# Kernel tuning notes

Measured on AMD Instinct MI355X. Metric: run time of the kernel, lower is better.

## Reference

```python
import jax, jax.numpy as jnp
import numpy as np


def setup_inputs() -> dict:
    key = jax.random.key(0)
    ks = jax.random.split(key, 24)
    N, C, D_IN, HID, EMB = 8192, 4096, 32, 128, 128
    s = 0.05
    inp = {
        "cand_feat": jax.random.normal(ks[0], (1, C, D_IN), jnp.float32),
        "graph_pos": jax.random.uniform(ks[1], (N, 3), jnp.float32),
        "graph_rad": jax.random.uniform(ks[2], (N,), jnp.float32) + 0.01,
        "L": jnp.ones((1,), jnp.float32),
        "adj": jax.random.uniform(ks[3], (N, N), jnp.float32),
        "mask": jax.random.randint(ks[4], (1, C), 0, 2, jnp.int32),
        # candidate encoder: 32 -> 128 -> 128
        "cW1": jax.random.normal(ks[5], (D_IN, 128), jnp.float32) * s,
        "cb1": jnp.zeros((128,), jnp.float32),
        "cW2": jax.random.normal(ks[6], (128, EMB), jnp.float32) * s,
        "cb2": jnp.zeros((EMB,), jnp.float32),
        # graph encoder input proj: 4 -> 128
        "gW0": jax.random.normal(ks[7], (4, HID), jnp.float32) * s,
        "gb0": jnp.zeros((HID,), jnp.float32),
        # 3 GNN layers: concat(2*HID) -> HID
        "gnnW": jax.random.normal(ks[8], (3, 2 * HID, HID), jnp.float32) * s,
        "gnnb": jnp.zeros((3, HID), jnp.float32),
        # output proj: 2*HID -> EMB
        "goW": jax.random.normal(ks[9], (2 * HID, EMB), jnp.float32) * s,
        "gob": jnp.zeros((EMB,), jnp.float32),
        # fusion: 2*EMB -> 256 -> 128 -> 1
        "fW1": jax.random.normal(ks[10], (2 * EMB, 256), jnp.float32) * s,
        "fb1": jnp.zeros((256,), jnp.float32),
        "fW2": jax.random.normal(ks[11], (256, 128), jnp.float32) * s,
        "fb2": jnp.zeros((128,), jnp.float32),
        "fW3": jax.random.normal(ks[12], (128, 1), jnp.float32) * s,
        "fb3": jnp.zeros((1,), jnp.float32),
    }
    return inp


def reference(cand_feat, graph_pos, graph_rad, L, adj, mask,
              cW1, cb1, cW2, cb2, gW0, gb0, gnnW, gnnb, goW, gob,
              fW1, fb1, fW2, fb2, fW3, fb3):
    relu = jax.nn.relu
    # ---- candidate encoder: [1, C, 32] -> [1, C, 128]
    cand_emb = relu(relu(cand_feat @ cW1 + cb1) @ cW2 + cb2)
    # ---- graph encoder ----
    node = jnp.concatenate([graph_pos / L, (graph_rad / jnp.max(graph_rad))[:, None]], axis=1)  # [N, 4]
    h = relu(node @ gW0 + gb0)  # [N, HID]
    deg = jnp.clip(jnp.sum(adj, axis=-1, keepdims=True), 1.0)  # [N, 1]
    for i in range(gnnW.shape[0]):
        agg = (adj @ h) / deg                       # degree-normalized aggregation
        h = relu(jnp.concatenate([h, agg], axis=-1) @ gnnW[i] + gnnb[i])
    h_glob = jnp.concatenate([jnp.max(h, axis=0), jnp.mean(h, axis=0)], axis=-1)  # [2*HID]
    graph_emb = h_glob @ goW + gob  # [EMB]
    # ---- fusion decoder ----
    g_exp = jnp.broadcast_to(graph_emb[None, None, :], cand_emb.shape)
    combined = jnp.concatenate([cand_emb, g_exp], axis=-1)  # [1, C, 2*EMB]
    scores = (relu(relu(combined @ fW1 + fb1) @ fW2 + fb2) @ fW3 + fb3)[..., 0]  # [1, C]
    return jnp.where(mask == 0, -jnp.inf, scores)
```

## Files before the change

kernel.cpp:

```cpp
#include <hip/hip_runtime.h>
#include <hip/hip_bf16.h>

constexpr int NN  = 8192;
constexpr int CC  = 4096;
constexpr int HD  = 128;
constexpr int KSPLIT = 8;
constexpr int KCHUNK = NN / KSPLIT;
constexpr int KSTEPS = KCHUNK / 64;

typedef __attribute__((ext_vector_type(8))) short bf16x8;
typedef __attribute__((ext_vector_type(4))) short s16x4;
typedef __attribute__((ext_vector_type(4))) float f32x4;

static __device__ __forceinline__ unsigned short f2bf(float f) {
  unsigned int u = __builtin_bit_cast(unsigned int, f);
  unsigned int lsb = (u >> 16) & 1u;
  u += 0x7fffu + lsb;
  return (unsigned short)(u >> 16);
}
static __device__ __forceinline__ float bf2f(unsigned short u) {
  return __builtin_bit_cast(float, ((unsigned int)u) << 16);
}

static __device__ __forceinline__ int swz(int r, int k) {
  return r * 128 + ((((k >> 3) ^ (r & 7))) << 4) + ((k & 7) * 2);
}

#define GL16(gp, lp)                                                              \
  __builtin_amdgcn_global_load_lds(                                               \
      (const __attribute__((address_space(1))) void*)(gp),                        \
      (__attribute__((address_space(3))) void*)(lp), 16, 0, 0)

__global__ __launch_bounds__(256) void k_radmax(const float* __restrict__ rad, float* out) {
  __shared__ float red[256];
  int t = threadIdx.x;
  float m = 0.0f;
  for (int i = t; i < NN; i += 256) m = fmaxf(m, rad[i]);
  red[t] = m; __syncthreads();
  for (int s = 128; s > 0; s >>= 1) {
    if (t < s) red[t] = fmaxf(red[t], red[t + s]);
    __syncthreads();
  }
  if (t == 0) out[0] = red[0];
}

__global__ __launch_bounds__(256) void k_h0(const float* __restrict__ pos, const float* __restrict__ rad,
                                            const float* __restrict__ Lp, const float* __restrict__ rmax,
                                            const float* __restrict__ gW0, const float* __restrict__ gb0,
                                            float* __restrict__ h, unsigned short* __restrict__ hT) {
  __shared__ __align__(16) unsigned short lt[128][72];
  int t = threadIdx.x;
  int i0 = blockIdx.x * 64;
  float invL = 1.0f / Lp[0];
  float invR = 1.0f / rmax[0];
  for (int rep = 0; rep < 32; ++rep) {
    int idx = rep * 256 + t;
    int il = idx >> 7, j = idx & 127;
    int i = i0 + il;
    float n0 = pos[i * 3 + 0] * invL, n1 = pos[i * 3 + 1] * invL, n2 = pos[i * 3 + 2] * invL;
    float n3 = rad[i] * invR;
    float v = gb0[j] + n0 * gW0[j] + n1 * gW0[128 + j] + n2 * gW0[256 + j] + n3 * gW0[384 + j];
    v = fmaxf(v, 0.0f);
    h[(size_t)i * HD + j] = v;
    lt[j][il] = f2bf(v);
  }
  __syncthreads();
  int j = t >> 1, half = t & 1;
  unsigned short* dst = hT + (size_t)j * NN + i0 + half * 32;
  const uint4* src = (const uint4*)&lt[j][half * 32];
  uint4* d4 = (uint4*)dst;
  d4[0] = src[0]; d4[1] = src[1]; d4[2] = src[2]; d4[3] = src[3];
}

#define COMPUTE(Ab, Bb)                                                              \
  _Pragma("unroll")                                                                  \
  for (int kk = 0; kk < 2; ++kk) {                                                   \
    int klo = kk * 32 + lk4;                                                         \
    bf16x8 afr[2];                                                                   \
    _Pragma("unroll")                                                                \
    for (int mi = 0; mi < 2; ++mi) {                                                 \
      int r = wr + mi * 16 + lr;                                                     \
      union { bf16x8 v; s16x4 p[2]; } ua;                                            \
      ua.p[0] = *(const s16x4*)((Ab) + swz(r, klo));                                 \
      ua.p[1] = *(const s16x4*)((Ab) + swz(r, klo + 16));                            \
      afr[mi] = ua.v;                                                                \
    }                                                                                \
    _Pragma("unroll")                                                                \
    for (int ni = 0; ni < 4; ++ni) {                                                 \
      int rn = wc + ni * 16 + lr;                                                    \
      union { bf16x8 v; s16x4 p[2]; } ub;                                            \
      ub.p[0] = *(const s16x4*)((Bb) + swz(rn, klo));                                \
      ub.p[1] = *(const s16x4*)((Bb) + swz(rn, klo + 16));                           \
      _Pragma("unroll")                                                              \
      for (int mi = 0; mi < 2; ++mi)                                                 \
        acc[mi][ni] = __builtin_amdgcn_mfma_f32_16x16x32_bf16(afr[mi], ub.v,         \
                                                              acc[mi][ni], 0, 0, 0); \
    }                                                                                \
  }

__global__ __launch_bounds__(256) void k_gemm23(const unsigned short* __restrict__ A16,
                                                const unsigned short* __restrict__ hT,
                                                unsigned short* __restrict__ part) {
  __shared__ __align__(16) char As[3][8192];
  __shared__ __align__(16) char Bs[3][16384];
  const int t = threadIdx.x, bm = blockIdx.x, ks = blockIdx.y;
  const int kbase = ks * KCHUNK;
  const int lane = t & 63, w = t >> 6;
  const int wr = (w >> 1) * 32, wc = (w & 1) * 64;
  const int lr = lane & 15, lk4 = (lane >> 4) * 4;
  const unsigned wb = (unsigned)__builtin_amdgcn_readfirstlane(w << 10);
  const int srow = t >> 3, sgl = (t & 7) ^ (srow & 7);

  const unsigned short* aS[2];
  const unsigned short* bS[4];
  #pragma unroll
  for (int it = 0; it < 2; ++it)
    aS[it] = A16 + (size_t)(bm * 64 + it * 32 + srow) * NN + kbase + sgl * 8;
  #pragma unroll
  for (int it = 0; it < 4; ++it)
    bS[it] = hT + (size_t)(it * 32 + srow) * NN + kbase + sgl * 8;

  f32x4 acc[2][4];
  #pragma unroll
  for (int a = 0; a < 2; ++a)
    #pragma unroll
    for (int b = 0; b < 4; ++b) acc[a][b] = f32x4{0.f, 0.f, 0.f, 0.f};

#define ISSUE23(s, d) do {                                 \
    GL16(aS[0] + (s) * 64, (char*)As[d] + wb);             \
    GL16(aS[1] + (s) * 64, (char*)As[d] + 4096 + wb);      \
    GL16(bS[0] + (s) * 64, (char*)Bs[d] + wb);             \
    GL16(bS[1] + (s) * 64, (char*)Bs[d] + 4096 + wb);      \
    GL16(bS[2] + (s) * 64, (char*)Bs[d] + 8192 + wb);      \
    GL16(bS[3] + (s) * 64, (char*)Bs[d] + 12288 + wb);     \
  } while (0)

  ISSUE23(0, 0);
  ISSUE23(1, 1);
  for (int step = 0; step < KSTEPS; ++step) {
    const int st = step % 3;
    if (step + 2 < KSTEPS) {
      ISSUE23(step + 2, (step + 2) % 3);
      asm volatile("s_waitcnt vmcnt(12)" ::: "memory");
    } else if (step + 1 < KSTEPS) {
      asm volatile("s_waitcnt vmcnt(6)" ::: "memory");
    } else {
      asm volatile("s_waitcnt vmcnt(0)" ::: "memory");
    }
    __builtin_amdgcn_s_barrier();
    __builtin_amdgcn_sched_barrier(0);
    COMPUTE(As[st], Bs[st]);
    __builtin_amdgcn_sched_barrier(0);
    __builtin_amdgcn_s_barrier();
  }
#undef ISSUE23

  unsigned short* outb = part + (size_t)ks * NN * HD;
  #pragma unroll
  for (int mi = 0; mi < 2; ++mi) {
    int rowb = bm * 64 + wr + mi * 16 + (lane >> 4) * 4;
    #pragma unroll
    for (int ni = 0; ni < 4; ++ni) {
      int col = wc + ni * 16 + lr;
      #pragma unroll
      for (int j = 0; j < 4; ++j)
        outb[(size_t)(rowb + j) * HD + col] = f2bf(acc[mi][ni][j]);
    }
  }
}

template <int WB, int DG>
__global__ __launch_bounds__(256) void k_gemm1(const float* __restrict__ A32,
                                               const unsigned short* __restrict__ hT,
                                               unsigned short* __restrict__ adjb,
                                               float* __restrict__ part_deg,
                                               unsigned short* __restrict__ part) {
  __shared__ __align__(16) char As[8192];
  __shared__ __align__(16) char Bs[16384];
  const int t = threadIdx.x, bm = blockIdx.x, ks = blockIdx.y;
  const int kbase = ks * KCHUNK;
  const int lane = t & 63, w = t >> 6;
  const int wr = (w >> 1) * 32, wc = (w & 1) * 64;
  const int lr = lane & 15, lk4 = (lane >> 4) * 4;
  const unsigned wb = (unsigned)__builtin_amdgcn_readfirstlane(w << 10);
  const int srow = t >> 3, sgl = (t & 7) ^ (srow & 7);

  const unsigned short* bS[4];
  #pragma unroll
  for (int it = 0; it < 4; ++it)
    bS[it] = hT + (size_t)(it * 32 + srow) * NN + kbase + sgl * 8;

  const int ar = t >> 2, agq = (t & 3) * 2;
  const float* a32Src = A32 + (size_t)(bm * 64 + ar) * NN + kbase + agq * 8;

  f32x4 acc[2][4];
  #pragma unroll
  for (int a = 0; a < 2; ++a)
    #pragma unroll
    for (int b = 0; b < 4; ++b) acc[a][b] = f32x4{0.f, 0.f, 0.f, 0.f};

  float rs = 0.f;
  for (int step = 0; step < KSTEPS; ++step) {
    __syncthreads();
    const float* src = a32Src + step * 64;
    float4 v0 = ((const float4*)src)[0], v1 = ((const float4*)src)[1];
    float4 v2 = ((const float4*)src)[2], v3 = ((const float4*)src)[3];
    union { unsigned short u[16]; uint4 q[2]; } pk;
    pk.u[0]  = f2bf(v0.x); pk.u[1]  = f2bf(v0.y); pk.u[2]  = f2bf(v0.z); pk.u[3]  = f2bf(v0.w);
    pk.u[4]  = f2bf(v1.x); pk.u[5]  = f2bf(v1.y); pk.u[6]  = f2bf(v1.z); pk.u[7]  = f2bf(v1.w);
    pk.u[8]  = f2bf(v2.x); pk.u[9]  = f2bf(v2.y); pk.u[10] = f2bf(v2.z); pk.u[11] = f2bf(v2.w);
    pk.u[12] = f2bf(v3.x); pk.u[13] = f2bf(v3.y); pk.u[14] = f2bf(v3.z); pk.u[15] = f2bf(v3.w);
    if (DG) rs += v0.x + v0.y + v0.z + v0.w + v1.x + v1.y + v1.z + v1.w
                + v2.x + v2.y + v2.z + v2.w + v3.x + v3.y + v3.z + v3.w;
    if (WB) {
      uint4* wdst = (uint4*)(adjb + (size_t)(bm * 64 + ar) * NN + kbase + step * 64 + agq * 8);
      wdst[0] = pk.q[0]; wdst[1] = pk.q[1];
    }
    *(uint4*)(As + ar * 128 + ((agq ^ (ar & 7)) << 4))       = pk.q[0];
    *(uint4*)(As + ar * 128 + (((agq + 1) ^ (ar & 7)) << 4)) = pk.q[1];
    #pragma unroll
    for (int it = 0; it < 4; ++it)
      GL16(bS[it] + step * 64, (char*)Bs + it * 4096 + wb);
    __syncthreads();
    COMPUTE(As, Bs);
  }

  if (DG) {
    float v = rs;
    v += __shfl_xor(v, 1);
    v += __shfl_xor(v, 2);
    if ((t & 3) == 0) part_deg[(size_t)ks * NN + bm * 64 + ar] = v;
  }

  unsigned short* outb = part + (size_t)ks * NN * HD;
  #pragma unroll
  for (int mi = 0; mi < 2; ++mi) {
    int rowb = bm * 64 + wr + mi * 16 + (lane >> 4) * 4;
    #pragma unroll
    for (int ni = 0; ni < 4; ++ni) {
      int col = wc + ni * 16 + lr;
      #pragma unroll
      for (int j = 0; j < 4; ++j)
        outb[(size_t)(rowb + j) * HD + col] = f2bf(acc[mi][ni][j]);
    }
  }
}

__global__ __launch_bounds__(256) void k_update(const unsigned short* __restrict__ part,
                                                const float* __restrict__ part_deg,
                                                const float* __restrict__ hin,
                                                const float* __restrict__ W, const float* __restrict__ bias,
                                                float* __restrict__ hout, unsigned short* __restrict__ hT,
                                                int last) {
  __shared__ float cc[16][256];
  __shared__ float degS[16];
  __shared__ __align__(16) unsigned short lt2[128][24];
  int t = threadIdx.x;
  int r0 = blockIdx.x * 16;
  if (t < 16) {
    float d = 0.f;
    for (int ks = 0; ks < KSPLIT; ++ks) d += part_deg[(size_t)ks * NN + r0 + t];
    degS[t] = fmaxf(d, 1.0f);
  }
  __syncthreads();
  for (int rep = 0; rep < 8; ++rep) {
    int idx = rep * 256 + t;
    int rl = idx >> 7, j = idx & 127;
    int row = r0 + rl;
    float s = 0.f;
    for (int ks = 0; ks < KSPLIT; ++ks)
      s += bf2f(part[((size_t)ks * NN + row) * HD + j]);
    cc[rl][128 + j] = s / degS[rl];
    cc[rl][j] = hin[(size_t)row * HD + j];
  }
  __syncthreads();
  int jo = t & 127, rbase = t >> 7;
  float accv[8];
  float bj = bias[jo];
  for (int rr = 0; rr < 8; ++rr) accv[rr] = bj;
  for (int jj = 0; jj < 256; ++jj) {
    float wv = W[jj * HD + jo];
    for (int rr = 0; rr < 8; ++rr) accv[rr] += cc[rbase + rr * 2][jj] * wv;
  }
  for (int rr = 0; rr < 8; ++rr) {
    int rl = rbase + rr * 2;
    float v = fmaxf(accv[rr], 0.f);
    hout[(size_t)(r0 + rl) * HD + jo] = v;
    if (!last) lt2[jo][rl] = f2bf(v);
  }
  if (!last) {
    __syncthreads();
    int j = t >> 1, half = t & 1;
    *(uint4*)(hT + (size_t)j * NN + r0 + half * 8) = *(const uint4*)&lt2[j][half * 8];
  }
}

__global__ __launch_bounds__(256) void k_pool(const float* __restrict__ h,
                                              float* __restrict__ pmax, float* __restrict__ psum) {
  int b = blockIdx.x, t = threadIdx.x;
  int j = t & 127, half = t >> 7;
  int r0 = b * 128 + half * 64;
  float mx = -1e30f, sm = 0.f;
  for (int r = r0; r < r0 + 64; ++r) {
    float v = h[(size_t)r * HD + j];
    mx = fmaxf(mx, v); sm += v;
  }
  __shared__ float lm[2][128], ls[2][128];
  lm[half][j] = mx; ls[half][j] = sm;
  __syncthreads();
  if (half == 0) {
    pmax[b * 128 + j] = fmaxf(lm[0][j], lm[1][j]);
    psum[b * 128 + j] = ls[0][j] + ls[1][j];
  }
}

__global__ __launch_bounds__(256) void k_glob(const float* __restrict__ pmax, const float* __restrict__ psum,
                                              const float* __restrict__ goW, const float* __restrict__ gob,
                                              float* __restrict__ ge) {
  __shared__ float hg[256];
  int t = threadIdx.x;
  int j = t & 127, which = t >> 7;
  if (which == 0) {
    float m = -1e30f;
    for (int b = 0; b < 64; ++b) m = fmaxf(m, pmax[b * 128 + j]);
    hg[j] = m;
  } else {
    float s = 0.f;
    for (int b = 0; b < 64; ++b) s += psum[b * 128 + j];
    hg[128 + j] = s * (1.0f / (float)NN);
  }
  __syncthreads();
  if (t < 128) {
    float s = gob[t];
    for (int jj = 0; jj < 256; ++jj) s += hg[jj] * goW[jj * HD + t];
    ge[t] = s;
  }
}

__global__ __launch_bounds__(256) void k_fusion(const float* __restrict__ cand, const float* __restrict__ ge,
                                                const int* __restrict__ mask,
                                                const float* __restrict__ cW1, const float* __restrict__ cb1,
                                                const float* __restrict__ cW2, const float* __restrict__ cb2,
                                                const float* __restrict__ fW1, const float* __restrict__ fb1,
                                                const float* __restrict__ fW2, const float* __restrict__ fb2,
                                                const float* __restrict__ fW3, const float* __restrict__ fb3,
                                                float* __restrict__ out) {
  __shared__ float x[16][32];
  __shared__ float t1[16][128];
  __shared__ float t2[16][128];
  __shared__ float u1[16][256];
  __shared__ float u2[16][129];
  __shared__ float geL[128];
  int t = threadIdx.x;
  int c0 = blockIdx.x * 16;
  if (t < 128) geL[t] = ge[t];
  for (int rep = 0; rep < 2; ++rep) {
    int idx = rep * 256 + t;
    int cl = idx >> 5, d = idx & 31;
    x[cl][d] = cand[(size_t)(c0 + cl) * 32 + d];
  }
  __syncthreads();
  {
    int j = t & 127, cg = (t >> 7) * 8;
    float a[8]; float bj = cb1[j];
    for (int q = 0; q < 8; ++q) a[q] = bj;
    for (int d = 0; d < 32; ++d) {
      float wv = cW1[d * 128 + j];
      for (int q = 0; q < 8; ++q) a[q] += x[cg + q][d] * wv;
    }
    for (int q = 0; q < 8; ++q) t1[cg + q][j] = fmaxf(a[q], 0.f);
  }
  __syncthreads();
  {
    int j = t & 127, cg = (t >> 7) * 8;
    float a[8]; float bj = cb2[j];
    for (int q = 0; q < 8; ++q) a[q] = bj;
    for (int d = 0; d < 128; ++d) {
      float wv = cW2[d * 128 + j];
      for (int q = 0; q < 8; ++q) a[q] += t1[cg + q][d] * wv;
    }
    for (int q = 0; q < 8; ++q) t2[cg + q][j] = fmaxf(a[q], 0.f);
  }
  __syncthreads();
  {
    int jo = t;
    float gp = fb1[jo];
    for (int d = 0; d < 128; ++d) gp += geL[d] * fW1[(128 + d) * 256 + jo];
    float a[16];
    for (int q = 0; q < 16; ++q) a[q] = gp;
    for (int d = 0; d < 128; ++d) {
      float wv = fW1[d * 256 + jo];
      for (int q = 0; q < 16; ++q) a[q] += t2[q][d] * wv;
    }
    for (int q = 0; q < 16; ++q) u1[q][jo] = fmaxf(a[q], 0.f);
  }
  __syncthreads();
  {
    int j = t & 127, cg = (t >> 7) * 8;
    float a[8]; float bj = fb2[j];
    for (int q = 0; q < 8; ++q) a[q] = bj;
    for (int d = 0; d < 256; ++d) {
      float wv = fW2[d * 128 + j];
      for (int q = 0; q < 8; ++q) a[q] += u1[cg + q][d] * wv;
    }
    for (int q = 0; q < 8; ++q) u2[cg + q][j] = fmaxf(a[q], 0.f);
  }
  __syncthreads();
  if (t < 16) {
    int c = c0 + t;
    float s = fb3[0];
    for (int d = 0; d < 128; ++d) s += u2[t][d] * fW3[d];
    out[c] = (mask[c] == 0) ? -3.0e38f : s;
  }
}

extern "C" void kernel_launch(void* const* d_in, const int* in_sizes, int n_in,
                              void* d_out, int out_size, void* d_ws, size_t ws_size,
                              hipStream_t stream) {
  const float* cand = (const float*)d_in[0];
  const float* pos  = (const float*)d_in[1];
  const float* rad  = (const float*)d_in[2];
  const float* Lp   = (const float*)d_in[3];
  const float* adj  = (const float*)d_in[4];
  const int*   mask = (const int*)d_in[5];
  const float* cW1 = (const float*)d_in[6];
  const float* cb1 = (const float*)d_in[7];
  const float* cW2 = (const float*)d_in[8];
  const float* cb2 = (const float*)d_in[9];
  const float* gW0 = (const float*)d_in[10];
  const float* gb0 = (const float*)d_in[11];
  const float* gnnW = (const float*)d_in[12];
  const float* gnnb = (const float*)d_in[13];
  const float* goW = (const float*)d_in[14];
  const float* gob = (const float*)d_in[15];
  const float* fW1 = (const float*)d_in[16];
  const float* fb1 = (const float*)d_in[17];
  const float* fW2 = (const float*)d_in[18];
  const float* fb2 = (const float*)d_in[19];
  const float* fW3 = (const float*)d_in[20];
  const float* fb3 = (const float*)d_in[21];

  char* ws = (char*)d_ws;
  float* h           = (float*)ws;
  unsigned short* hT = (unsigned short*)(ws + (4ull << 20));
  float* rmax        = (float*)(ws + (6ull << 20));
  float* pmax        = (float*)(ws + (6ull << 20) + 4096);
  float* psum        = pmax + 64 * 128;
  float* ge          = psum + 64 * 128;
  float* part_deg    = (float*)(ws + (7ull << 20));
  unsigned short* part = (unsigned short*)(ws + (8ull << 20));
  unsigned short* adjb = (unsigned short*)(ws + (24ull << 20));

  bool big = ws_size >= (24ull << 20) + (size_t)NN * NN * 2;

  k_radmax<<<1, 256, 0, stream>>>(rad, rmax);
  k_h0<<<NN / 64, 256, 0, stream>>>(pos, rad, Lp, rmax, gW0, gb0, h, hT);

  dim3 g(NN / 64, KSPLIT);
  for (int l = 0; l < 3; ++l) {
    if (l == 0) {
      if (big) k_gemm1<1, 1><<<g, 256, 0, stream>>>(adj, hT, adjb, part_deg, part);
      else     k_gemm1<0, 1><<<g, 256, 0, stream>>>(adj, hT, nullptr, part_deg, part);
    } else {
      if (big) k_gemm23<<<g, 256, 0, stream>>>(adjb, hT, part);
      else     k_gemm1<0, 0><<<g, 256, 0, stream>>>(adj, hT, nullptr, nullptr, part);
    }
    k_update<<<NN / 16, 256, 0, stream>>>(part, part_deg, h,
                                          gnnW + l * 256 * HD, gnnb + l * HD, h, hT, l == 2);
  }
  k_pool<<<64, 256, 0, stream>>>(h, pmax, psum);
  k_glob<<<1, 256, 0, stream>>>(pmax, psum, goW, gob, ge);
  k_fusion<<<CC / 16, 256, 0, stream>>>(cand, ge, mask, cW1, cb1, cW2, cb2,
                                        fW1, fb1, fW2, fb2, fW3, fb3, (float*)d_out);
}
```

Measured before the change: 420.2 us.

## Stage GEMM epilogue through LDS, swizzle block order, drop triple-buffer pipeline

Both GEMM kernels now write their bf16 accumulator tile into shared memory and then copy it to global memory with coalesced 16-byte stores, replacing scattered 2-byte stores. The row-block index is remapped so that consecutive launched blocks are spread across the row range, which is meant to change cache and channel locality. k_gemm23 drops its three-stage async prefetch pipeline and uses a single buffer with syncthreads around each load. That reduces shared memory use and may raise occupancy, but it gives up the overlap between loads and MFMA compute.

```diff
diff --git a/kernel.cpp b/kernel.cpp
--- a/kernel.cpp
+++ b/kernel.cpp
@@ -98,16 +98,39 @@
     }                                                                                \
   }
 
+#define EPILOGUE(smem_, dst_)                                                        \
+  do {                                                                               \
+    __syncthreads();                                                                 \
+    unsigned short* pl = (unsigned short*)(smem_);                                   \
+    _Pragma("unroll")                                                                \
+    for (int mi = 0; mi < 2; ++mi)                                                   \
+      _Pragma("unroll")                                                              \
+      for (int ni = 0; ni < 4; ++ni)                                                 \
+        _Pragma("unroll")                                                            \
+        for (int j = 0; j < 4; ++j)                                                  \
+          pl[(wr + mi * 16 + kg * 4 + j) * 128 + wc + ni * 16 + lr] =                \
+              f2bf(acc[mi][ni][j]);                                                  \
+    __syncthreads();                                                                 \
+    uint4* gout = (uint4*)(dst_);                                                    \
+    const uint4* lsrc = (const uint4*)pl;                                            \
+    int bq = (t >> 2) * 16 + (t & 3);                                                \
+    _Pragma("unroll")                                                                \
+    for (int k = 0; k < 4; ++k) gout[bq + k * 4] = lsrc[bq + k * 4];                 \
+  } while (0)
+
 __global__ __launch_bounds__(256) void k_gemm23(const unsigned short* __restrict__ A16,
                                                 const unsigned short* __restrict__ hT,
                                                 unsigned short* __restrict__ part) {
-  __shared__ __align__(16) char As[3][8192];
-  __shared__ __align__(16) char Bs[3][16384];
-  const int t = threadIdx.x, bm = blockIdx.x, ks = blockIdx.y;
+  __shared__ __align__(16) char smem[24576];
+  char* As = smem;
+  char* Bs = smem + 8192;
+  const int t = threadIdx.x;
+  const int bm = ((blockIdx.x & 7) << 4) | (blockIdx.x >> 3);
+  const int ks = blockIdx.y;
   const int kbase = ks * KCHUNK;
   const int lane = t & 63, w = t >> 6;
   const int wr = (w >> 1) * 32, wc = (w & 1) * 64;
-  const int lr = lane & 15, lk4 = (lane >> 4) * 4;
+  const int lr = lane & 15, kg = lane >> 4, lk4 = kg * 4;
   const unsigned wb = (unsigned)__builtin_amdgcn_readfirstlane(w << 10);
   const int srow = t >> 3, sgl = (t & 7) ^ (srow & 7);
 
@@ -126,47 +149,19 @@
     #pragma unroll
     for (int b = 0; b < 4; ++b) acc[a][b] = f32x4{0.f, 0.f, 0.f, 0.f};
 
-#define ISSUE23(s, d) do {                                 \
-    GL16(aS[0] + (s) * 64, (char*)As[d] + wb);             \
-    GL16(aS[1] + (s) * 64, (char*)As[d] + 4096 + wb);      \
-    GL16(bS[0] + (s) * 64, (char*)Bs[d] + wb);             \
-    GL16(bS[1] + (s) * 64, (char*)Bs[d] + 4096 + wb);      \
-    GL16(bS[2] + (s) * 64, (char*)Bs[d] + 8192 + wb);      \
-    GL16(bS[3] + (s) * 64, (char*)Bs[d] + 12288 + wb);     \
-  } while (0)
-
-  ISSUE23(0, 0);
-  ISSUE23(1, 1);
   for (int step = 0; step < KSTEPS; ++step) {
-    const int st = step % 3;
-    if (step + 2 < KSTEPS) {
-      ISSUE23(step + 2, (step + 2) % 3);
-      asm volatile("s_waitcnt vmcnt(12)" ::: "memory");
-    } else if (step + 1 < KSTEPS) {
-      asm volatile("s_waitcnt vmcnt(6)" ::: "memory");
-    } else {
-      asm volatile("s_waitcnt vmcnt(0)" ::: "memory");
-    }
-    __builtin_amdgcn_s_barrier();
-    __builtin_amdgcn_sched_barrier(0);
-    COMPUTE(As[st], Bs[st]);
-    __builtin_amdgcn_sched_barrier(0);
-    __builtin_amdgcn_s_barrier();
-  }
-#undef ISSUE23
-
-  unsigned short* outb = part + (size_t)ks * NN * HD;
-  #pragma unroll
-  for (int mi = 0; mi < 2; ++mi) {
-    int rowb = bm * 64 + wr + mi * 16 + (lane >> 4) * 4;
-    #pragma unroll
-    for (int ni = 0; ni < 4; ++ni) {
-      int col = wc + ni * 16 + lr;
-      #pragma unroll
-      for (int j = 0; j < 4; ++j)
-        outb[(size_t)(rowb + j) * HD + col] = f2bf(acc[mi][ni][j]);
-    }
-  }
+    __syncthreads();
+    GL16(aS[0] + step * 64, As + wb);
+    GL16(aS[1] + step * 64, As + 4096 + wb);
+    GL16(bS[0] + step * 64, Bs + wb);
+    GL16(bS[1] + step * 64, Bs + 4096 + wb);
+    GL16(bS[2] + step * 64, Bs + 8192 + wb);
+    GL16(bS[3] + step * 64, Bs + 12288 + wb);
+    __syncthreads();
+    COMPUTE(As, Bs);
+  }
+
+  EPILOGUE(smem, part + (size_t)ks * NN * HD + (size_t)bm * 64 * HD);
 }
 
 template <int WB, int DG>
@@ -175,13 +170,16 @@
                                                unsigned short* __restrict__ adjb,
                                                float* __restrict__ part_deg,
                                                unsigned short* __restrict__ part) {
-  __shared__ __align__(16) char As[8192];
-  __shared__ __align__(16) char Bs[16384];
-  const int t = threadIdx.x, bm = blockIdx.x, ks = blockIdx.y;
+  __shared__ __align__(16) char smem[24576];
+  char* As = smem;
+  char* Bs = smem + 8192;
+  const int t = threadIdx.x;
+  const int bm = ((blockIdx.x & 7) << 4) | (blockIdx.x >> 3);
+  const int ks = blockIdx.y;
   const int kbase = ks * KCHUNK;
   const int lane = t & 63, w = t >> 6;
   const int wr = (w >> 1) * 32, wc = (w & 1) * 64;
-  const int lr = lane & 15, lk4 = (lane >> 4) * 4;
+  const int lr = lane & 15, kg = lane >> 4, lk4 = kg * 4;
   const unsigned wb = (unsigned)__builtin_amdgcn_readfirstlane(w << 10);
   const int srow = t >> 3, sgl = (t & 7) ^ (srow & 7);
 
@@ -220,7 +218,7 @@
     *(uint4*)(As + ar * 128 + (((agq + 1) ^ (ar & 7)) << 4)) = pk.q[1];
     #pragma unroll
     for (int it = 0; it < 4; ++it)
-      GL16(bS[it] + step * 64, (char*)Bs + it * 4096 + wb);
+      GL16(bS[it] + step * 64, Bs + it * 4096 + wb);
     __syncthreads();
     COMPUTE(As, Bs);
   }
@@ -232,18 +230,7 @@
     if ((t & 3) == 0) part_deg[(size_t)ks * NN + bm * 64 + ar] = v;
   }
 
-  unsigned short* outb = part + (size_t)ks * NN * HD;
-  #pragma unroll
-  for (int mi = 0; mi < 2; ++mi) {
-    int rowb = bm * 64 + wr + mi * 16 + (lane >> 4) * 4;
-    #pragma unroll
-    for (int ni = 0; ni < 4; ++ni) {
-      int col = wc + ni * 16 + lr;
-      #pragma unroll
-      for (int j = 0; j < 4; ++j)
-        outb[(size_t)(rowb + j) * HD + col] = f2bf(acc[mi][ni][j]);
-    }
-  }
+  EPILOGUE(smem, part + (size_t)ks * NN * HD + (size_t)bm * 64 * HD);
 }
 
 __global__ __launch_bounds__(256) void k_update(const unsigned short* __restrict__ part,
```

Result: faster. 407.6 us (-3.0%).
